# Kernel optimization log

Measured on AMD Instinct MI355X. Metric: run time of the kernel, lower is better.

The kernel has to match this reference:

```python
import jax, jax.numpy as jnp
import numpy as np

MARGIN = 0.2


def setup_inputs() -> dict:
    key = jax.random.key(0)
    k1, k2 = jax.random.split(key)
    B, D, C = 4096, 512, 512
    embeddings = jax.random.normal(k1, (B, D), dtype=jnp.float32)
    labels = jax.random.randint(k2, (B,), 0, C, dtype=jnp.int64)
    return {"embeddings": embeddings, "labels": labels}


def reference(embeddings, labels):
    B = embeddings.shape[0]
    # L2-normalize rows (eps matches torch F.normalize default 1e-12)
    norm = jnp.maximum(jnp.linalg.norm(embeddings, axis=1, keepdims=True), 1e-12)
    e = embeddings / norm
    # cosine distance matrix [B, B]
    dist = 1.0 - e @ e.T
    same = labels[:, None] == labels[None, :]
    eye = jnp.eye(B, dtype=bool)
    pos_mask = same & ~eye
    neg_mask = ~same
    # dist in [0, 2]; sentinels outside that range for masked reductions
    hardest_pos = jnp.max(jnp.where(pos_mask, dist, -1.0), axis=1)
    hardest_neg = jnp.min(jnp.where(neg_mask, dist, 3.0), axis=1)
    valid = jnp.any(pos_mask, axis=1) & jnp.any(neg_mask, axis=1)
    per_anchor = jax.nn.relu(hardest_pos - hardest_neg + MARGIN)
    loss_sum = jnp.sum(jnp.where(valid, per_anchor, 0.0))
    n_valid = jnp.maximum(jnp.sum(valid.astype(jnp.int32)), 1)
    return loss_sum / n_valid.astype(embeddings.dtype)
```

## Files before the change

kernel.cpp:

```cpp
#include <hip/hip_runtime.h>
#include <hip/hip_bf16.h>

#define BDIM 4096
#define DDIM 512
#define BT 256
#define BK 64
#define NKT (DDIM / BK)
#define NPAN (BDIM / BT)
#define GRIDX (NPAN * NPAN)

typedef __bf16 bf16x8 __attribute__((ext_vector_type(8)));
typedef float f32x4 __attribute__((ext_vector_type(4)));
typedef unsigned short ushort_t;

__device__ inline ushort_t f2bf(float f) {
  __hip_bfloat16 h = __float2bfloat16(f);
  return *reinterpret_cast<ushort_t*>(&h);
}

__device__ inline unsigned int enc_f32(float x) {
  unsigned int u = __float_as_uint(x);
  return (u & 0x80000000u) ? ~u : (u | 0x80000000u);
}
__device__ inline float dec_f32(unsigned int e) {
  unsigned int u = (e & 0x80000000u) ? (e ^ 0x80000000u) : ~e;
  return __uint_as_float(u);
}

__global__ __launch_bounds__(256) void norm_kernel(const float* __restrict__ x,
                                                   ushort_t* __restrict__ e,
                                                   unsigned int* __restrict__ minpos_e,
                                                   unsigned int* __restrict__ maxneg_e) {
  if (blockIdx.x == 0) {
    const unsigned int init_min = enc_f32(1e30f);
    const unsigned int init_max = enc_f32(-1e30f);
    for (int i = threadIdx.x; i < BDIM; i += 256) {
      minpos_e[i] = init_min;
      maxneg_e[i] = init_max;
    }
  }
  const int row  = blockIdx.x * 4 + (threadIdx.x >> 6);
  const int lane = threadIdx.x & 63;
  const float4* xr = reinterpret_cast<const float4*>(x + (size_t)row * DDIM);
  float4 v0 = xr[lane];
  float4 v1 = xr[lane + 64];
  float ss = v0.x*v0.x + v0.y*v0.y + v0.z*v0.z + v0.w*v0.w
           + v1.x*v1.x + v1.y*v1.y + v1.z*v1.z + v1.w*v1.w;
#pragma unroll
  for (int off = 32; off >= 1; off >>= 1) ss += __shfl_xor(ss, off);
  const float inv = 1.0f / fmaxf(sqrtf(ss), 1e-12f);

  ushort4 p0, p1;
  p0.x = f2bf(v0.x * inv); p0.y = f2bf(v0.y * inv);
  p0.z = f2bf(v0.z * inv); p0.w = f2bf(v0.w * inv);
  p1.x = f2bf(v1.x * inv); p1.y = f2bf(v1.y * inv);
  p1.z = f2bf(v1.z * inv); p1.w = f2bf(v1.w * inv);
  ushort4* er = reinterpret_cast<ushort4*>(e + (size_t)row * DDIM);
  er[lane]      = p0;
  er[lane + 64] = p1;
}

#define STAGE(buf, kt)                                                         \
  do {                                                                         \
    _Pragma("unroll")                                                          \
    for (int q = 0; q < 8; ++q) {                                              \
      const int off  = q * 8192 + tid * 16;                      \
      const int loff = off & 32767;                                            \
      const int row  = loff >> 7;                                              \
      const int kb   = loff & 127;                                             \
      const int pan  = (q < 4) ? Ibase : Jbase;                                \
      const char* src = (const char*)e + (size_t)(pan + row) * (DDIM * 2) +    \
                        (kt) * 128 + (kb ^ ((row & 7) << 4));                  \
      __builtin_amdgcn_global_load_lds(                                        \
          (const __attribute__((address_space(1))) void*)src,                  \
          (__attribute__((address_space(3))) void*)(&Blds[buf][off]),          \
          16, 0, 0);                                                           \
    }                                                                          \
  } while (0)

__global__ __launch_bounds__(512, 2) void gemm_reduce_kernel(
    const ushort_t* __restrict__ e, const int* __restrict__ labels,
    unsigned int* __restrict__ minpos_e, unsigned int* __restrict__ maxneg_e) {
  __shared__ __align__(16) char Blds[2][65536];
  __shared__ int Llab[512];

  const int tid  = threadIdx.x;
  const int wave = tid >> 6;
  const int lane = tid & 63;
  const int l15  = lane & 15;
  const int g    = lane >> 4;
  const int wr   = wave >> 2;
  const int wc   = wave & 3;

  const int bid  = blockIdx.x;
  const int sbid = (bid & 7) * (GRIDX / 8) + (bid >> 3);
  const int Ibase = (sbid >> 4) * BT;
  const int Jbase = (sbid & 15) * BT;

  if (tid < 256) Llab[tid] = labels[Ibase + tid];
  else           Llab[tid] = labels[Jbase + tid - 256];

  f32x4 acc[8][4];
#pragma unroll
  for (int m = 0; m < 8; ++m)
#pragma unroll
    for (int n = 0; n < 4; ++n) acc[m][n] = (f32x4){0.f, 0.f, 0.f, 0.f};

  STAGE(0, 0);
  __syncthreads();

  for (int kt = 0; kt < NKT; ++kt) {
    if (kt + 1 < NKT) STAGE((kt + 1) & 1, kt + 1);

    const char* Ab = Blds[kt & 1];
    const char* Bb = Blds[kt & 1] + 32768;
#pragma unroll
    for (int kk = 0; kk < 2; ++kk) {
      bf16x8 a[8], b[4];
#pragma unroll
      for (int m = 0; m < 8; ++m) {
        const int row = wr * 128 + m * 16 + l15;
        a[m] = *reinterpret_cast<const bf16x8*>(
            Ab + row * 128 + ((kk * 64 + g * 16) ^ ((row & 7) << 4)));
      }
#pragma unroll
      for (int n = 0; n < 4; ++n) {
        const int row = wc * 64 + n * 16 + l15;
        b[n] = *reinterpret_cast<const bf16x8*>(
            Bb + row * 128 + ((kk * 64 + g * 16) ^ ((row & 7) << 4)));
      }
#pragma unroll
      for (int m = 0; m < 8; ++m)
#pragma unroll
        for (int n = 0; n < 4; ++n)
          acc[m][n] = __builtin_amdgcn_mfma_f32_16x16x32_bf16(a[m], b[n],
                                                              acc[m][n], 0, 0, 0);
    }
    __syncthreads();
  }

  float cmp[4], cmx[4];
  int lj[4], gj[4];
#pragma unroll
  for (int n = 0; n < 4; ++n) {
    cmp[n] = 1e30f; cmx[n] = -1e30f;
    gj[n]  = Jbase + wc * 64 + n * 16 + l15;
    lj[n]  = Llab[256 + wc * 64 + n * 16 + l15];
  }
#pragma unroll
  for (int m = 0; m < 8; ++m) {
#pragma unroll
    for (int r = 0; r < 4; ++r) {
      const int rloc = wr * 128 + m * 16 + g * 4 + r;
      const int li   = Llab[rloc];
      const int gi   = Ibase + rloc;
#pragma unroll
      for (int n = 0; n < 4; ++n) {
        const float v = acc[m][n][r];
        if (li == lj[n]) {
          if (gi != gj[n]) cmp[n] = fminf(cmp[n], v);
        } else {
          cmx[n] = fmaxf(cmx[n], v);
        }
      }
    }
  }
#pragma unroll
  for (int off = 16; off <= 32; off <<= 1) {
#pragma unroll
    for (int n = 0; n < 4; ++n) {
      cmp[n] = fminf(cmp[n], __shfl_xor(cmp[n], off));
      cmx[n] = fmaxf(cmx[n], __shfl_xor(cmx[n], off));
    }
  }
  if (g == 0) {
#pragma unroll
    for (int n = 0; n < 4; ++n) {
      if (cmp[n] < 1e29f)  atomicMin(&minpos_e[gj[n]], enc_f32(cmp[n]));
      if (cmx[n] > -1e29f) atomicMax(&maxneg_e[gj[n]], enc_f32(cmx[n]));
    }
  }
}

__global__ __launch_bounds__(1024) void finalize_kernel(
    const unsigned int* __restrict__ minpos_e, const unsigned int* __restrict__ maxneg_e,
    float* __restrict__ out) {
  const int tid = threadIdx.x;
  float sum = 0.f;
  int cnt = 0;
  for (int row = tid; row < BDIM; row += 1024) {
    const float mp = dec_f32(minpos_e[row]);
    const float mn = dec_f32(maxneg_e[row]);
    if (mp < 1e29f && mn > -1e29f) {
      sum += fmaxf(0.f, mn - mp + 0.2f);
      cnt += 1;
    }
  }
#pragma unroll
  for (int off = 32; off >= 1; off >>= 1) {
    sum += __shfl_xor(sum, off);
    cnt += __shfl_xor(cnt, off);
  }
  __shared__ float wsum[16];
  __shared__ int   wcnt[16];
  const int wv = tid >> 6, ln = tid & 63;
  if (ln == 0) { wsum[wv] = sum; wcnt[wv] = cnt; }
  __syncthreads();
  if (tid == 0) {
    float S = 0.f; int C = 0;
    for (int w = 0; w < 16; ++w) { S += wsum[w]; C += wcnt[w]; }
    out[0] = S / (float)(C > 0 ? C : 1);
  }
}

extern "C" void kernel_launch(void* const* d_in, const int* in_sizes, int n_in,
                              void* d_out, int out_size, void* d_ws, size_t ws_size,
                              hipStream_t stream) {
  const float* x      = (const float*)d_in[0];
  const int*   labels = (const int*)d_in[1];
  float* out = (float*)d_out;

  char* ws = (char*)d_ws;
  ushort_t* e            = (ushort_t*)ws;
  unsigned int* minpos_e = (unsigned int*)(ws + (size_t)BDIM * DDIM * 2);
  unsigned int* maxneg_e = minpos_e + BDIM;

  norm_kernel<<<BDIM / 4, 256, 0, stream>>>(x, e, minpos_e, maxneg_e);
  gemm_reduce_kernel<<<GRIDX, 512, 0, stream>>>(e, labels, minpos_e, maxneg_e);
  finalize_kernel<<<1, 1024, 0, stream>>>(minpos_e, maxneg_e, out);
}
```

Before: 34.37 us.

## Triple-buffer GEMM K-loop with BK=32 and explicit vmcnt waits

```diff
diff --git a/kernel.cpp b/kernel.cpp
--- a/kernel.cpp
+++ b/kernel.cpp
@@ -4,7 +4,7 @@
 #define BDIM 4096
 #define DDIM 512
 #define BT 256
-#define BK 64
+#define BK 32
 #define NKT (DDIM / BK)
 #define NPAN (BDIM / BT)
 #define GRIDX (NPAN * NPAN)
@@ -12,6 +12,10 @@
 typedef __bf16 bf16x8 __attribute__((ext_vector_type(8)));
 typedef float f32x4 __attribute__((ext_vector_type(4)));
 typedef unsigned short ushort_t;
+
+#define WAITV4() asm volatile("s_waitcnt vmcnt(4)" ::: "memory")
+#define WAITV0() asm volatile("s_waitcnt vmcnt(0)" ::: "memory")
+#define BAR()    asm volatile("s_barrier" ::: "memory")
 
 __device__ inline ushort_t f2bf(float f) {
   __hip_bfloat16 h = __float2bfloat16(f);
@@ -60,28 +64,38 @@
   er[lane + 64] = p1;
 }
 
-#define STAGE(buf, kt)                                                         \
+#define STAGE(bi, kt)                                                          \
   do {                                                                         \
     _Pragma("unroll")                                                          \
-    for (int q = 0; q < 8; ++q) {                                              \
-      const int off  = q * 8192 + tid * 16;                      \
-      const int loff = off & 32767;                                            \
-      const int row  = loff >> 7;                                              \
-      const int kb   = loff & 127;                                             \
-      const int pan  = (q < 4) ? Ibase : Jbase;                                \
-      const char* src = (const char*)e + (size_t)(pan + row) * (DDIM * 2) +    \
-                        (kt) * 128 + (kb ^ ((row & 7) << 4));                  \
+    for (int q = 0; q < 2; ++q) {                           \
+      const int off = q * 8192 + tid * 16;                                     \
+      const int row = off >> 6;                                                \
+      const int gg  = (off >> 4) & 3;                                          \
+      const char* src = (const char*)e + (size_t)(Ibase + row) * (DDIM * 2) +  \
+                        (kt) * 64 + ((gg ^ ((row >> 1) & 3)) << 4);            \
       __builtin_amdgcn_global_load_lds(                                        \
           (const __attribute__((address_space(1))) void*)src,                  \
-          (__attribute__((address_space(3))) void*)(&Blds[buf][off]),          \
+          (__attribute__((address_space(3))) void*)(&Blds[bi][off]),           \
+          16, 0, 0);                                                           \
+    }                                                                          \
+    _Pragma("unroll")                                                          \
+    for (int q = 0; q < 2; ++q) {                           \
+      const int off = q * 8192 + tid * 16;                                     \
+      const int row = off >> 6;                                                \
+      const int gg  = (off >> 4) & 3;                                          \
+      const char* src = (const char*)e + (size_t)(Jbase + row) * (DDIM * 2) +  \
+                        (kt) * 64 + ((gg ^ ((row >> 1) & 3)) << 4);            \
+      __builtin_amdgcn_global_load_lds(                                        \
+          (const __attribute__((address_space(1))) void*)src,                  \
+          (__attribute__((address_space(3))) void*)(&Blds[bi][16384 + off]),   \
           16, 0, 0);                                                           \
     }                                                                          \
   } while (0)
 
-__global__ __launch_bounds__(512, 2) void gemm_reduce_kernel(
+__global__ __launch_bounds__(512, 1) void gemm_reduce_kernel(
     const ushort_t* __restrict__ e, const int* __restrict__ labels,
     unsigned int* __restrict__ minpos_e, unsigned int* __restrict__ maxneg_e) {
-  __shared__ __align__(16) char Blds[2][65536];
+  __shared__ __align__(16) char Blds[3][32768];
   __shared__ int Llab[512];
 
   const int tid  = threadIdx.x;
@@ -97,47 +111,52 @@
   const int Ibase = (sbid >> 4) * BT;
   const int Jbase = (sbid & 15) * BT;
 
+  f32x4 acc[8][4];
+#pragma unroll
+  for (int m = 0; m < 8; ++m)
+#pragma unroll
+    for (int n = 0; n < 4; ++n) acc[m][n] = (f32x4){0.f, 0.f, 0.f, 0.f};
+
+  STAGE(0, 0);
+  STAGE(1, 1);
+  WAITV4();
+  BAR();
+
+#pragma unroll
+  for (int kt = 0; kt < NKT; ++kt) {
+    if (kt + 2 < NKT) STAGE((kt + 2) % 3, kt + 2);
+
+    const char* Ab = Blds[kt % 3];
+    const char* Bb = Ab + 16384;
+    bf16x8 a[8], b[4];
+#pragma unroll
+    for (int m = 0; m < 8; ++m) {
+      const int row = wr * 128 + m * 16 + l15;
+      a[m] = *reinterpret_cast<const bf16x8*>(
+          Ab + row * 64 + ((g ^ ((row >> 1) & 3)) << 4));
+    }
+#pragma unroll
+    for (int n = 0; n < 4; ++n) {
+      const int row = wc * 64 + n * 16 + l15;
+      b[n] = *reinterpret_cast<const bf16x8*>(
+          Bb + row * 64 + ((g ^ ((row >> 1) & 3)) << 4));
+    }
+    __builtin_amdgcn_s_setprio(1);
+#pragma unroll
+    for (int m = 0; m < 8; ++m)
+#pragma unroll
+      for (int n = 0; n < 4; ++n)
+        acc[m][n] = __builtin_amdgcn_mfma_f32_16x16x32_bf16(a[m], b[n],
+                                                            acc[m][n], 0, 0, 0);
+    __builtin_amdgcn_s_setprio(0);
+
+    if (kt + 2 < NKT) { WAITV4(); } else { WAITV0(); }
+    BAR();
+  }
+
   if (tid < 256) Llab[tid] = labels[Ibase + tid];
   else           Llab[tid] = labels[Jbase + tid - 256];
-
-  f32x4 acc[8][4];
-#pragma unroll
-  for (int m = 0; m < 8; ++m)
-#pragma unroll
-    for (int n = 0; n < 4; ++n) acc[m][n] = (f32x4){0.f, 0.f, 0.f, 0.f};
-
-  STAGE(0, 0);
   __syncthreads();
-
-  for (int kt = 0; kt < NKT; ++kt) {
-    if (kt + 1 < NKT) STAGE((kt + 1) & 1, kt + 1);
-
-    const char* Ab = Blds[kt & 1];
-    const char* Bb = Blds[kt & 1] + 32768;
-#pragma unroll
-    for (int kk = 0; kk < 2; ++kk) {
-      bf16x8 a[8], b[4];
-#pragma unroll
-      for (int m = 0; m < 8; ++m) {
-        const int row = wr * 128 + m * 16 + l15;
-        a[m] = *reinterpret_cast<const bf16x8*>(
-            Ab + row * 128 + ((kk * 64 + g * 16) ^ ((row & 7) << 4)));
-      }
-#pragma unroll
-      for (int n = 0; n < 4; ++n) {
-        const int row = wc * 64 + n * 16 + l15;
-        b[n] = *reinterpret_cast<const bf16x8*>(
-            Bb + row * 128 + ((kk * 64 + g * 16) ^ ((row & 7) << 4)));
-      }
-#pragma unroll
-      for (int m = 0; m < 8; ++m)
-#pragma unroll
-        for (int n = 0; n < 4; ++n)
-          acc[m][n] = __builtin_amdgcn_mfma_f32_16x16x32_bf16(a[m], b[n],
-                                                              acc[m][n], 0, 0, 0);
-    }
-    __syncthreads();
-  }
 
   float cmp[4], cmx[4];
   int lj[4], gj[4];
```

Result: no change. 34.64 us (+0.8%).
